# Optimization experiments

Measured on AMD Instinct MI355X. Metric: run time of the kernel, lower is better.

The kernel has to match this reference:

```python
import jax, jax.numpy as jnp
import numpy as np

B, C, H, W = 16, 512, 96, 96
CQK = C // 8


def setup_inputs() -> dict:
    key = jax.random.key(0)
    ks = jax.random.split(key, 8)
    s = 0.05  # keep projections / logits in a numerically sane range
    return {
        "x": jax.random.normal(ks[0], (B, C, H, W), jnp.float32),
        "Wq": jax.random.normal(ks[1], (CQK, C), jnp.float32) * s,
        "bq": jax.random.normal(ks[2], (CQK,), jnp.float32) * s,
        "Wk": jax.random.normal(ks[3], (CQK, C), jnp.float32) * s,
        "bk": jax.random.normal(ks[4], (CQK,), jnp.float32) * s,
        "Wv": jax.random.normal(ks[5], (C, C), jnp.float32) * s,
        "bv": jax.random.normal(ks[6], (C,), jnp.float32) * s,
        "gamma": jax.random.normal(ks[7], (1,), jnp.float32),
    }


def reference(x, Wq, bq, Wk, bk, Wv, bv, gamma):
    # 1x1 convs are per-pixel GEMMs
    q = jnp.einsum("bchw,oc->bohw", x, Wq) + bq[None, :, None, None]
    k = jnp.einsum("bchw,oc->bohw", x, Wk) + bk[None, :, None, None]
    v = jnp.einsum("bchw,oc->bohw", x, Wv) + bv[None, :, None, None]

    h = x.shape[2]
    # column affinities: query at (h,w) vs keys at (u,w)  -> [B,H,H,W]
    eH = jnp.einsum("bchw,bcuw->buhw", q, k)
    # exclude the center pixel from the column set (ca_forward uses H-1 column entries)
    center = jnp.arange(h)[:, None] == jnp.arange(h)[None, :]  # [u,h]
    eH = jnp.where(center[None, :, :, None], -jnp.inf, eH)
    # row affinities: query at (h,w) vs keys at (h,v) -> [B,W,H,W]
    eW = jnp.einsum("bchw,bchv->bvhw", q, k)

    energy = jnp.concatenate([eH, eW], axis=1)      # [B, H+W, H, W]
    att = jax.nn.softmax(energy, axis=1)
    aH, aW = att[:, :h], att[:, h:]

    # criss-cross aggregation (ca_map)
    out = jnp.einsum("buhw,bcuw->bchw", aH, v) + jnp.einsum("bvhw,bchv->bchw", aW, v)
    return gamma[0] * out + x
```

## Files before the change

### kernel.cpp

```cpp
#include <hip/hip_runtime.h>
#include <hip/hip_bf16.h>
#include <stdint.h>

#define BB 16
#define CC 512
#define CQK 64
#define HH 96
#define WW 96
#define HW (HH*WW)
#define NPIX (BB*HW)

typedef float f32x4 __attribute__((ext_vector_type(4)));
typedef short s16x8 __attribute__((ext_vector_type(8)));

__device__ __forceinline__ unsigned short f2bf(float f){
    unsigned u = __float_as_uint(f);
    unsigned r = (u + 0x7FFFu + ((u >> 16) & 1u)) >> 16;
    return (unsigned short)r;
}
__device__ __forceinline__ float bf2f(unsigned short h){
    return __uint_as_float(((unsigned)h) << 16);
}
__device__ __forceinline__ void gload16(const void* g, void* l){
    __builtin_amdgcn_global_load_lds((const __attribute__((address_space(1))) unsigned int*)g,
                                     (__attribute__((address_space(3))) unsigned int*)l, 16, 0, 0);
}

__global__ __launch_bounds__(256) void k_prep(const float* __restrict__ Wq, const float* __restrict__ Wk,
                                              const float* __restrict__ Wv, unsigned short* __restrict__ Wqkv,
                                              const float* __restrict__ x,
                                              unsigned short* __restrict__ xT,
                                              unsigned short* __restrict__ xbf){
    __shared__ float tile[64][65];
    int bid = blockIdx.x, t = threadIdx.x;
    if (bid < 640){
        const float* src = (bid < 64) ? (Wq + (size_t)bid*512)
                         : (bid < 128) ? (Wk + (size_t)(bid-64)*512)
                                       : (Wv + (size_t)(bid-128)*512);
        unsigned short* dst = Wqkv + (size_t)bid*512;
        for (int c = t; c < 512; c += 256) dst[c] = f2bf(src[c]);
        return;
    }
    int r = bid - 640;
    int nt = r % 144, ct = (r/144) & 7, b = r / 1152;
    const float* xb = x + ((size_t)(b*CC + ct*64))*HW + (size_t)nt*64;
    unsigned short* d2 = xbf + ((size_t)(b*CC + ct*64))*HW + (size_t)nt*64;
    #pragma unroll
    for (int s = 0; s < 4; s++){
        int idx = s*256 + t;
        int ci = idx >> 4, n4 = (idx & 15)*4;
        f32x4 vv = *(const f32x4*)(xb + (size_t)ci*HW + n4);
        *(f32x4*)(&tile[ci][n4]) = vv;
        ushort4 u; u.x=f2bf(vv[0]); u.y=f2bf(vv[1]); u.z=f2bf(vv[2]); u.w=f2bf(vv[3]);
        *(ushort4*)(d2 + (size_t)ci*HW + n4) = u;
    }
    __syncthreads();
    unsigned short* dst = xT + ((size_t)b*HW + (size_t)nt*64)*512 + ct*64;
    #pragma unroll
    for (int s = 0; s < 4; s++){
        int idx = s*256 + t;
        int ni = idx >> 4, c0 = (idx & 15)*4;
        ushort4 u;
        u.x = f2bf(tile[c0  ][ni]); u.y = f2bf(tile[c0+1][ni]);
        u.z = f2bf(tile[c0+2][ni]); u.w = f2bf(tile[c0+3][ni]);
        *(ushort4*)(dst + (size_t)ni*512 + c0) = u;
    }
}

__device__ __forceinline__ void stage_tiles8(const unsigned short* Ag, const unsigned short* Bg,
                                             unsigned short* As, unsigned short* Bs,
                                             int wv, int kt){
    #pragma unroll
    for (int s = 0; s < 2; s++){
        int chunk = wv*2 + s;
        gload16(Ag + (size_t)chunk*8*512 + (size_t)kt*64, As + chunk*512);
        gload16(Bg + (size_t)chunk*8*512 + (size_t)kt*64, Bs + chunk*512);
    }
}

__global__ __launch_bounds__(512) void k_gemm(const unsigned short* __restrict__ Wqkv,
                                              const unsigned short* __restrict__ xT,
                                              const float* __restrict__ bq, const float* __restrict__ bk,
                                              const float* __restrict__ bv,
                                              unsigned short* __restrict__ q_t,
                                              unsigned short* __restrict__ k_t,
                                              unsigned short* __restrict__ v){
    __shared__ unsigned short As[2][128*64];
    __shared__ unsigned short Bs[2][128*64];
    int b = blockIdx.z, mt = blockIdx.y, nt = blockIdx.x;
    int t = threadIdx.x, wv = t >> 6, lane = t & 63;
    int wr = wv >> 2, wc = wv & 3;
    const unsigned short* Ag = Wqkv + (size_t)(mt*128)*512
                               + (size_t)(lane>>3)*512 + (size_t)(((lane&7) ^ (lane>>3))*8);
    const unsigned short* Bg = xT + ((size_t)b*HW + (size_t)nt*128)*512
                               + (size_t)(lane>>3)*512 + (size_t)(((lane&7) ^ (lane>>3))*8);
    f32x4 acc[4][2] = {};
    stage_tiles8(Ag, Bg, As[0], Bs[0], wv, 0);
    stage_tiles8(Ag, Bg, As[1], Bs[1], wv, 1);
    #pragma unroll
    for (int kt = 0; kt < 8; kt++){
        int cur = kt & 1;
        if (kt < 7) asm volatile("s_waitcnt vmcnt(4)" ::: "memory");
        else        asm volatile("s_waitcnt vmcnt(0)" ::: "memory");
        __builtin_amdgcn_s_barrier();
        asm volatile("" ::: "memory");
        __builtin_amdgcn_s_setprio(1);
        #pragma unroll
        for (int kk = 0; kk < 2; kk++){
            int xr = (((kk*4 + (lane>>4)) ^ (lane&7)) << 3);
            s16x8 af[4], bfr[2];
            #pragma unroll
            for (int i = 0; i < 4; i++) af[i]  = *(const s16x8*)(&As[cur][(wr*64 + i*16 + (lane&15))*64 + xr]);
            #pragma unroll
            for (int j = 0; j < 2; j++) bfr[j] = *(const s16x8*)(&Bs[cur][(wc*32 + j*16 + (lane&15))*64 + xr]);
            #pragma unroll
            for (int i = 0; i < 4; i++)
                #pragma unroll
                for (int j = 0; j < 2; j++)
                    acc[i][j] = __builtin_amdgcn_mfma_f32_16x16x32_bf16(af[i], bfr[j], acc[i][j], 0, 0, 0);
        }
        __builtin_amdgcn_s_setprio(0);
        asm volatile("" ::: "memory");
        __builtin_amdgcn_s_barrier();
        asm volatile("" ::: "memory");
        if (kt < 6) stage_tiles8(Ag, Bg, As[cur], Bs[cur], wv, kt+2);
    }
    if (mt == 0){
        const float* bias = (wr == 0) ? bq : bk;
        unsigned short* dst = (wr == 0) ? q_t : k_t;
        #pragma unroll
        for (int i = 0; i < 4; i++){
            int m0 = i*16 + (lane >> 4)*4;
            f32x4 bb = *(const f32x4*)(bias + m0);
            #pragma unroll
            for (int j = 0; j < 2; j++){
                int n = nt*128 + wc*32 + j*16 + (lane & 15);
                ushort4 u;
                u.x = f2bf(acc[i][j][0] + bb[0]);
                u.y = f2bf(acc[i][j][1] + bb[1]);
                u.z = f2bf(acc[i][j][2] + bb[2]);
                u.w = f2bf(acc[i][j][3] + bb[3]);
                *(ushort4*)(dst + ((size_t)b*HW + n)*64 + m0) = u;
            }
        }
    } else {
        #pragma unroll
        for (int i = 0; i < 4; i++){
            int c0 = (mt-1)*128 + wr*64 + i*16 + (lane >> 4)*4;
            f32x4 bb = *(const f32x4*)(bv + c0);
            #pragma unroll
            for (int j = 0; j < 2; j++){
                int n = nt*128 + wc*32 + j*16 + (lane & 15);
                #pragma unroll
                for (int r = 0; r < 4; r++)
                    v[((size_t)b*CC + c0 + r)*HW + n] = f2bf(acc[i][j][r] + bb[r]);
            }
        }
    }
}

__global__ __launch_bounds__(256) void k_vt_energy(const unsigned short* __restrict__ v,
                                                   unsigned short* __restrict__ vT,
                                                   const unsigned short* __restrict__ q_t,
                                                   const unsigned short* __restrict__ k_t,
                                                   unsigned short* __restrict__ E){
    __shared__ char smem[96*97*4];
    int bid = blockIdx.x, t = threadIdx.x;
    if (bid < 8192){
        unsigned int (*tile)[97] = (unsigned int(*)[97])smem;
        int b = bid >> 9, c = bid & 511;
        const unsigned short* src = v + ((size_t)b*CC + c)*HW;
        unsigned short* dst = vT + ((size_t)b*CC + c)*HW;
        for (int idx = t; idx < HW; idx += 256){
            tile[idx/96][idx%96] = src[idx];
        }
        __syncthreads();
        for (int idx = t; idx < HW; idx += 256){
            int w = idx/96, h = idx%96;
            dst[idx] = (unsigned short)tile[h][w];
        }
        return;
    }
    int idx2 = bid - 8192;
    int y = idx2 % 192, b = idx2 / 192;
    unsigned short* qs = (unsigned short*)smem;
    unsigned short* ks = qs + 96*72;
    int wv = t >> 6, lane = t & 63;
    int wrow = wv >> 1, wcol = wv & 1;
    int modeW = (y >= 96);
    size_t base, rstride;
    if (!modeW){ base = ((size_t)b*HW + y)*64;                 rstride = (size_t)96*64; }
    else       { base = ((size_t)b*HW + (size_t)(y-96)*96)*64; rstride = 64; }
    #pragma unroll
    for (int s = 0; s < 3; s++){
        int chunk = s*256 + t;
        int row = chunk >> 3, c8 = chunk & 7;
        *(s16x8*)(&qs[row*72 + c8*8]) = *(const s16x8*)(q_t + base + (size_t)row*rstride + c8*8);
        *(s16x8*)(&ks[row*72 + c8*8]) = *(const s16x8*)(k_t + base + (size_t)row*rstride + c8*8);
    }
    __syncthreads();
    f32x4 acc[3][3] = {};
    #pragma unroll
    for (int kk = 0; kk < 2; kk++){
        int ko = kk*32 + (lane >> 4)*8;
        s16x8 af[3], bfr[3];
        #pragma unroll
        for (int i = 0; i < 3; i++) af[i]  = *(const s16x8*)(&qs[(wrow*48 + i*16 + (lane&15))*72 + ko]);
        #pragma unroll
        for (int j = 0; j < 3; j++) bfr[j] = *(const s16x8*)(&ks[(wcol*48 + j*16 + (lane&15))*72 + ko]);
        #pragma unroll
        for (int i = 0; i < 3; i++)
            #pragma unroll
            for (int j = 0; j < 3; j++)
                acc[i][j] = __builtin_amdgcn_mfma_f32_16x16x32_bf16(af[i], bfr[j], acc[i][j], 0, 0, 0);
    }
    #pragma unroll
    for (int i = 0; i < 3; i++){
        #pragma unroll
        for (int j = 0; j < 3; j++){
            #pragma unroll
            for (int r = 0; r < 4; r++){
                int row = wrow*48 + i*16 + (lane >> 4)*4 + r;
                int col = wcol*48 + j*16 + (lane & 15);
                float val = acc[i][j][r];
                size_t pix; int jcol;
                if (!modeW){ pix = (size_t)b*HW + (size_t)row*96 + y; jcol = col;
                             if (row == col) val = -1e30f; }
                else       { pix = (size_t)b*HW + (size_t)(y-96)*96 + row; jcol = 96 + col; }
                E[pix*192 + jcol] = f2bf(val);
            }
        }
    }
}

__global__ __launch_bounds__(256) void k_softmax(const unsigned short* __restrict__ E,
                                                 unsigned short* __restrict__ att){
    int t = threadIdx.x;
    int g = t & 7;
    size_t pix = (size_t)blockIdx.x*32 + (t >> 3);
    const unsigned short* e = E + pix*192 + g*24;
    s16x8 a[3];
    a[0] = *(const s16x8*)(e);
    a[1] = *(const s16x8*)(e + 8);
    a[2] = *(const s16x8*)(e + 16);
    float vals[24];
    float m = -3e38f;
    #pragma unroll
    for (int s = 0; s < 3; s++)
        #pragma unroll
        for (int q = 0; q < 8; q++){
            float f = bf2f((unsigned short)a[s][q]);
            vals[s*8+q] = f;
            m = fmaxf(m, f);
        }
    #pragma unroll
    for (int d = 1; d < 8; d <<= 1) m = fmaxf(m, __shfl_xor(m, d, 64));
    float sum = 0.f;
    #pragma unroll
    for (int q = 0; q < 24; q++){ vals[q] = __expf(vals[q] - m); sum += vals[q]; }
    #pragma unroll
    for (int d = 1; d < 8; d <<= 1) sum += __shfl_xor(sum, d, 64);
    float inv = 1.0f / sum;
    unsigned short* o = att + pix*192 + g*24;
    #pragma unroll
    for (int s = 0; s < 3; s++){
        s16x8 u;
        #pragma unroll
        for (int q = 0; q < 8; q++) u[q] = (short)f2bf(vals[s*8+q]*inv);
        *(s16x8*)(o + s*8) = u;
    }
}

__global__ __launch_bounds__(256, 4) void k_agg(const unsigned short* __restrict__ v,
                                                const unsigned short* __restrict__ vT,
                                                const unsigned short* __restrict__ att,
                                                unsigned short* __restrict__ outH,
                                                unsigned short* __restrict__ outW){
    __shared__ unsigned short As[64*104];
    __shared__ unsigned short Bs[96*104];
    int b = blockIdx.y, xx = blockIdx.x;
    int mh = xx / 192, r2 = xx % 192, modeW = r2 / 96, y = r2 % 96;
    int t = threadIdx.x, wvv = t >> 6, lane = t & 63;
    const unsigned short* Ag = (modeW ? v : vT) + ((size_t)b*CC + (size_t)mh*64)*HW + (size_t)y*96;
    const unsigned short* Bg; size_t bstride;
    if (!modeW){ Bg = att + ((size_t)b*HW + y)*192;                 bstride = (size_t)96*192; }
    else       { Bg = att + ((size_t)b*HW + (size_t)y*96)*192 + 96; bstride = 192; }
    #pragma unroll
    for (int s = 0; s < 3; s++){
        int chunk = s*256 + t;
        int row = chunk/12, c8 = chunk%12;
        *(s16x8*)(&As[row*104 + c8*8]) = *(const s16x8*)(Ag + (size_t)row*HW + c8*8);
    }
    #pragma unroll
    for (int s = 0; s < 5; s++){
        int chunk = s*256 + t;
        if (chunk < 1152){
            int row = chunk/12, c8 = chunk%12;
            *(s16x8*)(&Bs[row*104 + c8*8]) = *(const s16x8*)(Bg + (size_t)row*bstride + c8*8);
        }
    }
    __syncthreads();
    f32x4 acc[6] = {};
    #pragma unroll
    for (int kk = 0; kk < 3; kk++){
        int ko = kk*32 + (lane >> 4)*8;
        s16x8 af, bfr[6];
        af = *(const s16x8*)(&As[(wvv*16 + (lane&15))*104 + ko]);
        #pragma unroll
        for (int j = 0; j < 6; j++) bfr[j] = *(const s16x8*)(&Bs[(j*16 + (lane&15))*104 + ko]);
        #pragma unroll
        for (int j = 0; j < 6; j++)
            acc[j] = __builtin_amdgcn_mfma_f32_16x16x32_bf16(af, bfr[j], acc[j], 0, 0, 0);
    }
    __syncthreads();
    #pragma unroll
    for (int j = 0; j < 6; j++){
        int col = j*16 + (lane & 15);
        #pragma unroll
        for (int r = 0; r < 4; r++){
            int cl = wvv*16 + (lane >> 4)*4 + r;
            As[cl*104 + col] = f2bf(acc[j][r]);
        }
    }
    __syncthreads();
    unsigned short* OUT = modeW ? outW : outH;
    size_t obase = ((size_t)b*CC + (size_t)mh*64)*HW + (size_t)y*96;
    #pragma unroll
    for (int s = 0; s < 3; s++){
        int chunk = s*256 + t;
        int row = chunk/12, c8 = chunk%12;
        *(s16x8*)(OUT + obase + (size_t)row*HW + c8*8) = *(const s16x8*)(&As[row*104 + c8*8]);
    }
}

__global__ __launch_bounds__(256) void k_combine(const unsigned short* __restrict__ outH,
                                                 const unsigned short* __restrict__ outW,
                                                 const unsigned short* __restrict__ xbf,
                                                 const float* __restrict__ gamma,
                                                 float* __restrict__ out){
    __shared__ float tile[96][97];
    int b = blockIdx.y, c = blockIdx.x, t = threadIdx.x;
    const unsigned short* hp = outH + ((size_t)b*CC + c)*HW;
    #pragma unroll
    for (int s = 0; s < 9; s++){
        int idx = s*1024 + t*4;
        ushort4 u = *(const ushort4*)(hp + idx);
        int r = idx/96, cc = idx%96;
        tile[r][cc] = bf2f(u.x); tile[r][cc+1] = bf2f(u.y);
        tile[r][cc+2] = bf2f(u.z); tile[r][cc+3] = bf2f(u.w);
    }
    __syncthreads();
    float g = gamma[0];
    size_t base = ((size_t)b*CC + c)*HW;
    #pragma unroll
    for (int s = 0; s < 9; s++){
        int idx = s*1024 + t*4;
        ushort4 uw = *(const ushort4*)(outW + base + idx);
        ushort4 ux = *(const ushort4*)(xbf + base + idx);
        int h = idx/96, w = idx%96;
        f32x4 o;
        o[0] = g*(bf2f(uw.x) + tile[w  ][h]) + bf2f(ux.x);
        o[1] = g*(bf2f(uw.y) + tile[w+1][h]) + bf2f(ux.y);
        o[2] = g*(bf2f(uw.z) + tile[w+2][h]) + bf2f(ux.z);
        o[3] = g*(bf2f(uw.w) + tile[w+3][h]) + bf2f(ux.w);
        *(f32x4*)(out + base + idx) = o;
    }
}

extern "C" void kernel_launch(void* const* d_in, const int* in_sizes, int n_in,
                              void* d_out, int out_size, void* d_ws, size_t ws_size,
                              hipStream_t stream){
    const float* x     = (const float*)d_in[0];
    const float* Wq    = (const float*)d_in[1];
    const float* bq    = (const float*)d_in[2];
    const float* Wk    = (const float*)d_in[3];
    const float* bk    = (const float*)d_in[4];
    const float* Wv    = (const float*)d_in[5];
    const float* bv    = (const float*)d_in[6];
    const float* gamma = (const float*)d_in[7];

    constexpr size_t SZ_BIG = (size_t)BB*CC*HW*2;
    constexpr size_t SZ_QK  = (size_t)BB*HW*64*2;
    constexpr size_t SZ_ATT = (size_t)BB*HW*192*2;

    char* ws = (char*)d_ws;
    unsigned short* xT   = (unsigned short*)(ws);
    unsigned short* v    = (unsigned short*)(ws + SZ_BIG);
    unsigned short* xbf  = (unsigned short*)(ws + 2*SZ_BIG);
    unsigned short* q_t  = (unsigned short*)(ws + 3*SZ_BIG);
    unsigned short* k_t  = (unsigned short*)(ws + 3*SZ_BIG + SZ_QK);
    unsigned short* att  = (unsigned short*)(ws + 3*SZ_BIG + 2*SZ_QK);
    unsigned short* Wqkv = (unsigned short*)(ws + 3*SZ_BIG + 2*SZ_QK + SZ_ATT);

    unsigned short* E    = (unsigned short*)d_out;
    unsigned short* vT   = (unsigned short*)((char*)d_out + SZ_BIG);
    float*          out  = (float*)d_out;
    unsigned short* outH = xT;
    unsigned short* outW = v;

    k_prep      <<<dim3(19072),    dim3(256), 0, stream>>>(Wq, Wk, Wv, Wqkv, x, xT, xbf);
    k_gemm      <<<dim3(72, 5, 16),dim3(512), 0, stream>>>(Wqkv, xT, bq, bk, bv, q_t, k_t, v);
    k_vt_energy <<<dim3(11264),    dim3(256), 0, stream>>>(v, vT, q_t, k_t, E);
    k_softmax   <<<dim3(4608),     dim3(256), 0, stream>>>(E, att);
    k_agg       <<<dim3(1536, 16), dim3(256), 0, stream>>>(v, vT, att, outH, outW);
    k_combine   <<<dim3(512, 16),  dim3(256), 0, stream>>>(outH, outW, xbf, gamma, out);
}
```

Baseline: 681.9 us.

## Pipeline k_agg over four rows with double-buffered LDS, vectorize vT transpose

```diff
diff --git a/kernel.cpp b/kernel.cpp
--- a/kernel.cpp
+++ b/kernel.cpp
@@ -164,20 +164,37 @@
                                                    const unsigned short* __restrict__ q_t,
                                                    const unsigned short* __restrict__ k_t,
                                                    unsigned short* __restrict__ E){
-    __shared__ char smem[96*97*4];
+    __shared__ char smem[96*72*2*2];
     int bid = blockIdx.x, t = threadIdx.x;
     if (bid < 8192){
-        unsigned int (*tile)[97] = (unsigned int(*)[97])smem;
+        unsigned short* tile = (unsigned short*)smem;
         int b = bid >> 9, c = bid & 511;
         const unsigned short* src = v + ((size_t)b*CC + c)*HW;
         unsigned short* dst = vT + ((size_t)b*CC + c)*HW;
-        for (int idx = t; idx < HW; idx += 256){
-            tile[idx/96][idx%96] = src[idx];
+        #pragma unroll
+        for (int s = 0; s < 5; s++){
+            int chunk = s*256 + t;
+            if (chunk < 1152){
+                int row = chunk/12, g = chunk%12;
+                int pg = g ^ ((row>>3)&7);
+                *(s16x8*)(&tile[row*128 + pg*8]) = *(const s16x8*)(src + chunk*8);
+            }
         }
         __syncthreads();
-        for (int idx = t; idx < HW; idx += 256){
-            int w = idx/96, h = idx%96;
-            dst[idx] = (unsigned short)tile[h][w];
+        #pragma unroll
+        for (int s = 0; s < 5; s++){
+            int c2 = s*256 + t;
+            if (c2 < 1152){
+                int w = c2/12, h0 = (c2%12)*8;
+                s16x8 u;
+                #pragma unroll
+                for (int k = 0; k < 8; k++){
+                    int h = h0 + k;
+                    int gw = (w>>3) ^ ((h>>3)&7);
+                    u[k] = (short)tile[h*128 + gw*8 + (w&7)];
+                }
+                *(s16x8*)(dst + (size_t)w*96 + h0) = u;
+            }
         }
         return;
     }
@@ -271,66 +288,102 @@
     }
 }
 
-__global__ __launch_bounds__(256, 4) void k_agg(const unsigned short* __restrict__ v,
+__global__ __launch_bounds__(256, 2) void k_agg(const unsigned short* __restrict__ v,
                                                 const unsigned short* __restrict__ vT,
                                                 const unsigned short* __restrict__ att,
                                                 unsigned short* __restrict__ outH,
                                                 unsigned short* __restrict__ outW){
-    __shared__ unsigned short As[64*104];
-    __shared__ unsigned short Bs[96*104];
+    __shared__ unsigned short As[2][64*104];
+    __shared__ unsigned short Bs[2][96*104];
+    __shared__ unsigned short Os[64*104];
     int b = blockIdx.y, xx = blockIdx.x;
-    int mh = xx / 192, r2 = xx % 192, modeW = r2 / 96, y = r2 % 96;
+    int combo = xx / 24, ygrp = xx % 24;
+    int mh = combo >> 1, modeW = combo & 1;
+    int y0 = ygrp * 4;
     int t = threadIdx.x, wvv = t >> 6, lane = t & 63;
-    const unsigned short* Ag = (modeW ? v : vT) + ((size_t)b*CC + (size_t)mh*64)*HW + (size_t)y*96;
-    const unsigned short* Bg; size_t bstride;
-    if (!modeW){ Bg = att + ((size_t)b*HW + y)*192;                 bstride = (size_t)96*192; }
-    else       { Bg = att + ((size_t)b*HW + (size_t)y*96)*192 + 96; bstride = 192; }
-    #pragma unroll
-    for (int s = 0; s < 3; s++){
-        int chunk = s*256 + t;
-        int row = chunk/12, c8 = chunk%12;
-        *(s16x8*)(&As[row*104 + c8*8]) = *(const s16x8*)(Ag + (size_t)row*HW + c8*8);
-    }
-    #pragma unroll
-    for (int s = 0; s < 5; s++){
-        int chunk = s*256 + t;
-        if (chunk < 1152){
+    const unsigned short* Abase = (modeW ? v : vT) + ((size_t)b*CC + (size_t)mh*64)*HW;
+    size_t bstride = modeW ? 192 : (size_t)96*192;
+    unsigned short* OUT = modeW ? outW : outH;
+
+    int arow[3], ac8[3];
+    #pragma unroll
+    for (int s = 0; s < 3; s++){ int ch = s*256 + t; arow[s] = ch/12; ac8[s] = ch%12; }
+    int brow[5], bc8[5]; bool bok[5];
+    #pragma unroll
+    for (int s = 0; s < 5; s++){ int ch = s*256 + t; bok[s] = ch < 1152;
+        int cc = bok[s] ? ch : 0; brow[s] = cc/12; bc8[s] = cc%12; }
+
+    s16x8 ra[3], rb[5];
+    #define ISSUE_LOADS(y) { \
+        const unsigned short* Ag = Abase + (size_t)(y)*96; \
+        const unsigned short* Bg = modeW ? (att + ((size_t)b*HW + (size_t)(y)*96)*192 + 96) \
+                                         : (att + ((size_t)b*HW + (y))*192); \
+        _Pragma("unroll") \
+        for (int s = 0; s < 3; s++) ra[s] = *(const s16x8*)(Ag + (size_t)arow[s]*HW + ac8[s]*8); \
+        _Pragma("unroll") \
+        for (int s = 0; s < 5; s++) if (bok[s]) rb[s] = *(const s16x8*)(Bg + (size_t)brow[s]*bstride + bc8[s]*8); \
+        asm volatile("" ::: "memory"); }
+    #define WRITE_LDS(buf) { \
+        _Pragma("unroll") \
+        for (int s = 0; s < 3; s++) *(s16x8*)(&As[buf][arow[s]*104 + ac8[s]*8]) = ra[s]; \
+        _Pragma("unroll") \
+        for (int s = 0; s < 5; s++) if (bok[s]) *(s16x8*)(&Bs[buf][brow[s]*104 + bc8[s]*8]) = rb[s]; \
+        asm volatile("" ::: "memory"); }
+
+    ISSUE_LOADS(y0);
+    WRITE_LDS(0);
+    ISSUE_LOADS(y0+1);
+    asm volatile("s_waitcnt lgkmcnt(0)" ::: "memory");
+    __builtin_amdgcn_s_barrier();
+    asm volatile("" ::: "memory");
+
+    #pragma unroll
+    for (int i = 0; i < 4; i++){
+        int cur = i & 1;
+        int y = y0 + i;
+        f32x4 acc[6] = {};
+        __builtin_amdgcn_s_setprio(1);
+        #pragma unroll
+        for (int kk = 0; kk < 3; kk++){
+            int ko = kk*32 + (lane >> 4)*8;
+            s16x8 af, bfr[6];
+            af = *(const s16x8*)(&As[cur][(wvv*16 + (lane&15))*104 + ko]);
+            #pragma unroll
+            for (int j = 0; j < 6; j++) bfr[j] = *(const s16x8*)(&Bs[cur][(j*16 + (lane&15))*104 + ko]);
+            #pragma unroll
+            for (int j = 0; j < 6; j++)
+                acc[j] = __builtin_amdgcn_mfma_f32_16x16x32_bf16(af, bfr[j], acc[j], 0, 0, 0);
+        }
+        __builtin_amdgcn_s_setprio(0);
+        #pragma unroll
+        for (int j = 0; j < 6; j++){
+            int col = j*16 + (lane & 15);
+            #pragma unroll
+            for (int r = 0; r < 4; r++){
+                int cl = wvv*16 + (lane >> 4)*4 + r;
+                Os[cl*104 + col] = f2bf(acc[j][r]);
+            }
+        }
+        asm volatile("s_waitcnt lgkmcnt(0)" ::: "memory");
+        __builtin_amdgcn_s_barrier();
+        asm volatile("" ::: "memory");
+        size_t obase = ((size_t)b*CC + (size_t)mh*64)*HW + (size_t)y*96;
+        #pragma unroll
+        for (int s = 0; s < 3; s++){
+            int chunk = s*256 + t;
             int row = chunk/12, c8 = chunk%12;
-            *(s16x8*)(&Bs[row*104 + c8*8]) = *(const s16x8*)(Bg + (size_t)row*bstride + c8*8);
-        }
-    }
-    __syncthreads();
-    f32x4 acc[6] = {};
-    #pragma unroll
-    for (int kk = 0; kk < 3; kk++){
-        int ko = kk*32 + (lane >> 4)*8;
-        s16x8 af, bfr[6];
-        af = *(const s16x8*)(&As[(wvv*16 + (lane&15))*104 + ko]);
-        #pragma unroll
-        for (int j = 0; j < 6; j++) bfr[j] = *(const s16x8*)(&Bs[(j*16 + (lane&15))*104 + ko]);
-        #pragma unroll
-        for (int j = 0; j < 6; j++)
-            acc[j] = __builtin_amdgcn_mfma_f32_16x16x32_bf16(af, bfr[j], acc[j], 0, 0, 0);
-    }
-    __syncthreads();
-    #pragma unroll
-    for (int j = 0; j < 6; j++){
-        int col = j*16 + (lane & 15);
-        #pragma unroll
-        for (int r = 0; r < 4; r++){
-            int cl = wvv*16 + (lane >> 4)*4 + r;
-            As[cl*104 + col] = f2bf(acc[j][r]);
-        }
-    }
-    __syncthreads();
-    unsigned short* OUT = modeW ? outW : outH;
-    size_t obase = ((size_t)b*CC + (size_t)mh*64)*HW + (size_t)y*96;
-    #pragma unroll
-    for (int s = 0; s < 3; s++){
-        int chunk = s*256 + t;
-        int row = chunk/12, c8 = chunk%12;
-        *(s16x8*)(OUT + obase + (size_t)row*HW + c8*8) = *(const s16x8*)(&As[row*104 + c8*8]);
-    }
+            *(s16x8*)(OUT + obase + (size_t)row*HW + c8*8) = *(const s16x8*)(&Os[row*104 + c8*8]);
+        }
+        if (i < 3){
+            WRITE_LDS(cur^1);
+            if (i < 2) ISSUE_LOADS(y0+i+2);
+            asm volatile("s_waitcnt lgkmcnt(0)" ::: "memory");
+            __builtin_amdgcn_s_barrier();
+            asm volatile("" ::: "memory");
+        }
+    }
+    #undef ISSUE_LOADS
+    #undef WRITE_LDS
 }
 
 __global__ __launch_bounds__(256) void k_combine(const unsigned short* __restrict__ outH,
@@ -402,6 +455,6 @@
     k_gemm      <<<dim3(72, 5, 16),dim3(512), 0, stream>>>(Wqkv, xT, bq, bk, bv, q_t, k_t, v);
     k_vt_energy <<<dim3(11264),    dim3(256), 0, stream>>>(v, vT, q_t, k_t, E);
     k_softmax   <<<dim3(4608),     dim3(256), 0, stream>>>(E, att);
-    k_agg       <<<dim3(1536, 16), dim3(256), 0, stream>>>(v, vT, att, outH, outW);
+    k_agg       <<<dim3(384, 16),  dim3(256), 0, stream>>>(v, vT, att, outH, outW);
     k_combine   <<<dim3(512, 16),  dim3(256), 0, stream>>>(outH, outW, xbf, gamma, out);
 }
```

Measured after the change: 662.1 us (median of 2 runs). 2.9% less time.
